# Performance work log

Measured on AMD Instinct MI355X. Metric: run time of the kernel, lower is better.

Reference implementation:

```python
import jax, jax.numpy as jnp
import numpy as np

ATT = 16          # attention_size -> window = 2*ATT+1 = 33
HID = 512         # middle hidden size


def setup_inputs() -> dict:
    key = jax.random.key(0)
    ks = jax.random.split(key, 7)
    B, S, D_IN = 4, 2048, 256
    def xav(k, shape):
        fan_in, fan_out = shape[0], shape[1]
        std = np.sqrt(2.0 / (fan_in + fan_out))
        return jax.random.normal(k, shape, dtype=jnp.float32) * std
    return {
        "x": jax.random.normal(ks[0], (B, S, D_IN), dtype=jnp.float32),
        "Wq": xav(ks[1], (HID, HID)),
        "Wk": xav(ks[2], (HID, HID)),
        "Wv": xav(ks[3], (HID, HID)),
        "W0": xav(ks[4], (D_IN, HID)),
        "b0": jnp.zeros((1, 1, HID), dtype=jnp.float32),
        "W1": xav(ks[5], (HID, HID)),
        "b1": jnp.zeros((1, 1, HID), dtype=jnp.float32),
        "Wout": xav(ks[6], (HID, 2)),
        "bout": jnp.zeros((1, 1, 2), dtype=jnp.float32),
    }


def _local_windows(h, A):
    # h: [B, S, H] -> nei: [B, S, 2A+1, H], nei[b,t,j] = h[b, t+A-j] (zero padded)
    S = h.shape[1]
    padded = jnp.pad(h, ((0, 0), (A, A), (0, 0)))
    t = jnp.arange(S)[:, None]
    j = jnp.arange(2 * A + 1)[None, :]
    idx = t + 2 * A - j  # padded index of h[t + A - j]
    return padded[:, idx, :]


def reference(x, Wq, Wk, Wv, W0, b0, W1, b1, Wout, bout):
    scale = jnp.float32(np.sqrt(float(HID)))
    # pre-attention MLP layer(s)
    h = jax.nn.relu(x @ W0 + b0)                       # [B,S,H]
    nei = _local_windows(h, ATT)                       # [B,S,W,H]
    q = h @ Wq                                         # [B,S,H]
    k = nei @ Wk                                       # [B,S,W,H]
    v = nei @ Wv                                       # [B,S,W,H]
    dist = jnp.einsum('bsd,bswd->bsw', q, k) / scale   # [B,S,W]
    attn = jax.nn.softmax(dist, axis=-1)               # [B,S,W]
    ctx = jnp.einsum('bsw,bswd->bsd', attn, v)         # [B,S,H]
    # post-attention MLP layers
    h2 = jax.nn.relu(ctx @ W1 + b1)
    out = h2 @ Wout + bout                             # [B,S,2]
    return out, attn[:, :, None, :]  # attn shape [B,S,1,W] as in torch
```

## Files before the change

kernel.cpp:

```cpp
#include <hip/hip_runtime.h>

#define S_LEN 2048
#define HID 512
#define DIN 256
#define WIN 33
#define MROWS 8192
#define VTB 2080
#define VTROW 8320
#define SCALE_INV 0.04419417382415922f

typedef __attribute__((ext_vector_type(8))) short short8;
typedef __attribute__((ext_vector_type(4))) float f32x4;

__device__ __forceinline__ unsigned short f2bf(float f) {
    unsigned u = __builtin_bit_cast(unsigned, f);
    u += 0x7fffu + ((u >> 16) & 1u);
    return (unsigned short)(u >> 16);
}
__device__ __forceinline__ float bf2f(unsigned short h) {
    unsigned u = ((unsigned)h) << 16;
    return __builtin_bit_cast(float, u);
}
__device__ __forceinline__ void gl_lds16(const unsigned short* g, unsigned short* l) {
    __builtin_amdgcn_global_load_lds(
        (__attribute__((address_space(1))) unsigned int*)(g),
        (__attribute__((address_space(3))) unsigned int*)(l),
        16, 0, 0);
}

__global__ __launch_bounds__(256) void prep_kernel(
    const float* __restrict__ x,
    const float* __restrict__ Wq, const float* __restrict__ Wk,
    const float* __restrict__ Wv, const float* __restrict__ W0,
    const float* __restrict__ W1, const float* __restrict__ bout,
    unsigned short* __restrict__ xb, unsigned short* __restrict__ Wt0,
    unsigned short* __restrict__ Wtqkv, unsigned short* __restrict__ Wt1,
    unsigned short* __restrict__ Vt, float* __restrict__ outp)
{
    __shared__ float tile[32][33];
    const int blk = blockIdx.x, tid = threadIdx.x;
    if (blk < 2048) {
        int i = (blk * 256 + tid) * 4;
        float4 v = *(const float4*)(x + i);
        unsigned lo = (unsigned)f2bf(v.x) | ((unsigned)f2bf(v.y) << 16);
        unsigned hi = (unsigned)f2bf(v.z) | ((unsigned)f2bf(v.w) << 16);
        uint2 p; p.x = lo; p.y = hi;
        *(uint2*)(xb + i) = p;
    } else if (blk < 2064) {
        int i = ((blk - 2048) * 256 + tid) * 4;
        float4 o; o.x = bout[0]; o.y = bout[1]; o.z = bout[0]; o.w = bout[1];
        *(float4*)(outp + i) = o;
    } else if (blk < 2320) {
        int t = (blk - 2064) * 256 + tid;
        int v = t >> 7, s = t & 127;
        int b = s >> 5, p = s & 31;
        int off = (p < 16) ? p : (2048 + p);
        Vt[(size_t)v * VTROW + b * VTB + off] = 0;
    } else {
        int tt = blk - 2320;
        const float* in; unsigned short* out; int K, kt, nt;
        if (tt < 128) { in = W0; out = Wt0; K = DIN; kt = tt & 7; nt = tt >> 3; }
        else {
            int z = (tt - 128) >> 8, r = (tt - 128) & 255;
            kt = r & 15; nt = r >> 4; K = HID;
            if (z == 0)      { in = Wq; out = Wtqkv; }
            else if (z == 1) { in = Wk; out = Wtqkv + 512 * 512; }
            else if (z == 2) { in = Wv; out = Wtqkv + 2 * 512 * 512; }
            else             { in = W1; out = Wt1; }
        }
        int k0 = kt * 32, n0 = nt * 32;
        int tx = tid & 31, ty = tid >> 5;
        for (int j = 0; j < 32; j += 8)
            tile[ty + j][tx] = in[(size_t)(k0 + ty + j) * HID + n0 + tx];
        __syncthreads();
        for (int j = 0; j < 32; j += 8)
            out[(size_t)(n0 + ty + j) * K + k0 + tx] = f2bf(tile[tx][ty + j]);
    }
}

template<int K, int MODE>
__global__ __launch_bounds__(256) void gemm128_kernel(
    const unsigned short* __restrict__ A,
    const unsigned short* __restrict__ Bt,
    const float* __restrict__ bias,
    unsigned short* __restrict__ C0,
    unsigned short* __restrict__ C1,
    unsigned short* __restrict__ C2,
    const float* __restrict__ Wout,
    float* __restrict__ outp)
{
    __shared__ __align__(16) unsigned short SMEM[8192];
    const int tid = threadIdx.x;
    const int lane = tid & 63, wid = tid >> 6;
    const int bn = blockIdx.x, bm = blockIdx.y;
    const int wr = wid >> 1, wc = wid & 1;
    const int r16 = lane & 15, kq = lane >> 4;

    f32x4 acc[4][4] = {};

    const int c0 = tid, c1 = tid + 256;
    const unsigned short* aS0 = A + (size_t)(bm * 128 + (c0 & 127)) * K + (c0 >> 7) * 8;
    const unsigned short* aS1 = A + (size_t)(bm * 128 + (c1 & 127)) * K + (c1 >> 7) * 8;
    const unsigned short* bS0 = Bt + (size_t)(bn * 128 + (c0 & 127)) * K + (c0 >> 7) * 8;
    const unsigned short* bS1 = Bt + (size_t)(bn * 128 + (c1 & 127)) * K + (c1 >> 7) * 8;
    unsigned short* aD0 = SMEM + c0 * 8;
    unsigned short* aD1 = SMEM + c1 * 8;
    unsigned short* bD0 = SMEM + 4096 + c0 * 8;
    unsigned short* bD1 = SMEM + 4096 + c1 * 8;

    for (int kt = 0; kt < K / 32; ++kt) {
        gl_lds16(aS0 + kt * 32, aD0);
        gl_lds16(aS1 + kt * 32, aD1);
        gl_lds16(bS0 + kt * 32, bD0);
        gl_lds16(bS1 + kt * 32, bD1);
        __syncthreads();
        short8 af[4], bfr[4];
        #pragma unroll
        for (int mi = 0; mi < 4; ++mi)
            af[mi] = *(const short8*)(SMEM + kq * 1024 + (wr * 64 + mi * 16 + r16) * 8);
        #pragma unroll
        for (int ni = 0; ni < 4; ++ni)
            bfr[ni] = *(const short8*)(SMEM + 4096 + kq * 1024 + (wc * 64 + ni * 16 + r16) * 8);
        #pragma unroll
        for (int mi = 0; mi < 4; ++mi)
            #pragma unroll
            for (int ni = 0; ni < 4; ++ni)
                acc[mi][ni] = __builtin_amdgcn_mfma_f32_16x16x32_bf16(af[mi], bfr[ni], acc[mi][ni], 0, 0, 0);
        __syncthreads();
    }

    if constexpr (MODE == 0) {
        #pragma unroll
        for (int mi = 0; mi < 4; ++mi) {
            int row0 = bm * 128 + wr * 64 + mi * 16 + kq * 4;
            #pragma unroll
            for (int ni = 0; ni < 4; ++ni) {
                int col = bn * 128 + wc * 64 + ni * 16 + r16;
                float bv = bias[col];
                #pragma unroll
                for (int r = 0; r < 4; ++r) {
                    float v = fmaxf(acc[mi][ni][r] + bv, 0.0f);
                    C0[(size_t)(row0 + r) * HID + col] = f2bf(v);
                }
            }
        }
    } else if constexpr (MODE == 1) {
        if (bn < 8) {
            unsigned short* dst = (bn < 4) ? C0 : C1;
            int cb = (bn & 3) * 128 + wc * 64;
            #pragma unroll
            for (int mi = 0; mi < 4; ++mi) {
                int row0 = bm * 128 + wr * 64 + mi * 16 + kq * 4;
                #pragma unroll
                for (int ni = 0; ni < 4; ++ni) {
                    int col = cb + ni * 16 + r16;
                    #pragma unroll
                    for (int r = 0; r < 4; ++r)
                        dst[(size_t)(row0 + r) * HID + col] = f2bf(acc[mi][ni][r]);
                }
            }
        } else {
            const int bb  = (bm * 128) >> 11;
            const int tl0 = (bm * 128) & 2047;
            #pragma unroll
            for (int p = 0; p < 2; ++p) {
                if (wc == p) {
                    #pragma unroll
                    for (int mi = 0; mi < 4; ++mi) {
                        int ttw = wr * 64 + mi * 16 + kq * 4;
                        #pragma unroll
                        for (int ni = 0; ni < 4; ++ni) {
                            int vv = ni * 16 + r16;
                            unsigned lo = (unsigned)f2bf(acc[mi][ni][0]) | ((unsigned)f2bf(acc[mi][ni][1]) << 16);
                            unsigned hi = (unsigned)f2bf(acc[mi][ni][2]) | ((unsigned)f2bf(acc[mi][ni][3]) << 16);
                            uint2 pk; pk.x = lo; pk.y = hi;
                            *(uint2*)&SMEM[vv * 128 + (ttw ^ ((vv & 7) << 3))] = pk;
                        }
                    }
                }
                __syncthreads();
                #pragma unroll
                for (int it = 0; it < 4; ++it) {
                    int vv  = (tid >> 4) + it * 16;
                    int tt8 = (tid & 15) * 8;
                    uint4 q = *(const uint4*)&SMEM[vv * 128 + (tt8 ^ ((vv & 7) << 3))];
                    int vg = (bn - 8) * 128 + p * 64 + vv;
                    *(uint4*)(C2 + (size_t)vg * VTROW + bb * VTB + 16 + tl0 + tt8) = q;
                }
                __syncthreads();
            }
        }
    } else {
        float o0[16], o1[16];
        #pragma unroll
        for (int t2 = 0; t2 < 16; ++t2) { o0[t2] = 0.0f; o1[t2] = 0.0f; }
        #pragma unroll
        for (int ni = 0; ni < 4; ++ni) {
            int col = bn * 128 + wc * 64 + ni * 16 + r16;
            float bv = bias[col];
            float2 wv = *(const float2*)(Wout + col * 2);
            #pragma unroll
            for (int mi = 0; mi < 4; ++mi)
                #pragma unroll
                for (int r = 0; r < 4; ++r) {
                    float v = fmaxf(acc[mi][ni][r] + bv, 0.0f);
                    o0[mi * 4 + r] += v * wv.x;
                    o1[mi * 4 + r] += v * wv.y;
                }
        }
        #pragma unroll
        for (int s = 1; s < 16; s <<= 1)
            #pragma unroll
            for (int t2 = 0; t2 < 16; ++t2) {
                o0[t2] += __shfl_xor(o0[t2], s);
                o1[t2] += __shfl_xor(o1[t2], s);
            }
        if (r16 == 0) {
            #pragma unroll
            for (int mi = 0; mi < 4; ++mi)
                #pragma unroll
                for (int r = 0; r < 4; ++r) {
                    int row = bm * 128 + wr * 64 + mi * 16 + kq * 4 + r;
                    atomicAdd(&outp[(size_t)row * 2],     o0[mi * 4 + r]);
                    atomicAdd(&outp[(size_t)row * 2 + 1], o1[mi * 4 + r]);
                }
        }
    }
}

__global__ __launch_bounds__(256) void attn_kernel(
    const unsigned short* __restrict__ Qb,
    const unsigned short* __restrict__ Kb,
    const unsigned short* __restrict__ Vt,
    float* __restrict__ attn_out,
    unsigned short* __restrict__ ctx)
{
    __shared__ __align__(16) float Sl[4][32][66];
    __shared__ __align__(16) unsigned short Pl[32 * 64];
    const int tid = threadIdx.x;
    const int lane = tid & 63;
    const int w = tid >> 6;
    const int t0g = blockIdx.x * 32;
    const int b = t0g >> 11;
    const int t0 = t0g & 2047;
    const int r16 = lane & 15, kq = lane >> 4;

    f32x4 s[2][4] = {};
    const unsigned short* qbase = Qb + (size_t)t0g * HID + w * 128 + kq * 8;
    const unsigned short* kbase = Kb + (long)(t0g - 16) * HID + w * 128 + kq * 8;
    #pragma unroll
    for (int ks = 0; ks < 4; ++ks) {
        short8 a0 = *(const short8*)(qbase + (size_t)r16 * HID + ks * 32);
        short8 a1 = *(const short8*)(qbase + (size_t)(16 + r16) * HID + ks * 32);
        #pragma unroll
        for (int ni = 0; ni < 4; ++ni) {
            short8 bf = *(const short8*)(kbase + (size_t)(ni * 16 + r16) * HID + ks * 32);
            s[0][ni] = __builtin_amdgcn_mfma_f32_16x16x32_bf16(a0, bf, s[0][ni], 0, 0, 0);
            s[1][ni] = __builtin_amdgcn_mfma_f32_16x16x32_bf16(a1, bf, s[1][ni], 0, 0, 0);
        }
    }
    #pragma unroll
    for (int mi = 0; mi < 2; ++mi)
        #pragma unroll
        for (int ni = 0; ni < 4; ++ni)
            #pragma unroll
            for (int r = 0; r < 4; ++r)
                Sl[w][mi * 16 + kq * 4 + r][ni * 16 + r16] = s[mi][ni][r];
    __syncthreads();

    {
        const int i = tid >> 3;
        const int c8 = (tid & 7) * 8;
        float sv[8];
        #pragma unroll
        for (int cc = 0; cc < 8; ++cc) {
            float a = Sl[0][i][c8 + cc] + Sl[1][i][c8 + cc]
                    + Sl[2][i][c8 + cc] + Sl[3][i][c8 + cc];
            int m = c8 + cc;
            bool inb = (m >= i) && (m <= i + 32);
            int krow = t0 + m - 16;
            bool inseq = (krow >= 0) && (krow < S_LEN);
            sv[cc] = inb ? (inseq ? a * SCALE_INV : 0.0f) : -INFINITY;
        }
        float mx = sv[0];
        #pragma unroll
        for (int cc = 1; cc < 8; ++cc) mx = fmaxf(mx, sv[cc]);
        mx = fmaxf(mx, __shfl_xor(mx, 1));
        mx = fmaxf(mx, __shfl_xor(mx, 2));
        mx = fmaxf(mx, __shfl_xor(mx, 4));
        float es = 0.0f;
        #pragma unroll
        for (int cc = 0; cc < 8; ++cc) { sv[cc] = __expf(sv[cc] - mx); es += sv[cc]; }
        es += __shfl_xor(es, 1);
        es += __shfl_xor(es, 2);
        es += __shfl_xor(es, 4);
        float inv = 1.0f / es;
        unsigned short pb[8];
        #pragma unroll
        for (int cc = 0; cc < 8; ++cc) {
            float p = sv[cc] * inv;
            pb[cc] = f2bf(p);
            int m = c8 + cc;
            if (m >= i && m <= i + 32)
                attn_out[(size_t)(t0g + i) * WIN + (i + 32 - m)] = p;
        }
        uint4 pk;
        pk.x = (unsigned)pb[0] | ((unsigned)pb[1] << 16);
        pk.y = (unsigned)pb[2] | ((unsigned)pb[3] << 16);
        pk.z = (unsigned)pb[4] | ((unsigned)pb[5] << 16);
        pk.w = (unsigned)pb[6] | ((unsigned)pb[7] << 16);
        *(uint4*)((char*)Pl + i * 128 + ((c8 * 2) ^ ((i & 7) << 4))) = pk;
    }
    __syncthreads();

    f32x4 c[2][8] = {};
    const char* plb = (const char*)Pl;
    const unsigned short* vtb = Vt + (size_t)b * VTB + t0;
    #pragma unroll
    for (int ks = 0; ks < 2; ++ks) {
        int cb = ks * 64 + kq * 16;
        short8 a0 = *(const short8*)(plb + r16 * 128 + (cb ^ ((r16 & 7) << 4)));
        short8 a1 = *(const short8*)(plb + (16 + r16) * 128 + (cb ^ ((r16 & 7) << 4)));
        #pragma unroll
        for (int nd = 0; nd < 8; ++nd) {
            const unsigned short* vp = vtb + (size_t)(w * 128 + nd * 16 + r16) * VTROW + ks * 32 + kq * 8;
            short8 bf = *(const short8*)vp;
            c[0][nd] = __builtin_amdgcn_mfma_f32_16x16x32_bf16(a0, bf, c[0][nd], 0, 0, 0);
            c[1][nd] = __builtin_amdgcn_mfma_f32_16x16x32_bf16(a1, bf, c[1][nd], 0, 0, 0);
        }
    }
    #pragma unroll
    for (int mi = 0; mi < 2; ++mi) {
        int row0 = t0g + mi * 16 + kq * 4;
        #pragma unroll
        for (int nd = 0; nd < 8; ++nd) {
            int col = w * 128 + nd * 16 + r16;
            #pragma unroll
            for (int r = 0; r < 4; ++r)
                ctx[(size_t)(row0 + r) * HID + col] = f2bf(c[mi][nd][r]);
        }
    }
}

extern "C" void kernel_launch(void* const* d_in, const int* in_sizes, int n_in,
                              void* d_out, int out_size, void* d_ws, size_t ws_size,
                              hipStream_t stream)
{
    const float* x    = (const float*)d_in[0];
    const float* Wq   = (const float*)d_in[1];
    const float* Wk   = (const float*)d_in[2];
    const float* Wv   = (const float*)d_in[3];
    const float* W0   = (const float*)d_in[4];
    const float* b0   = (const float*)d_in[5];
    const float* W1   = (const float*)d_in[6];
    const float* b1   = (const float*)d_in[7];
    const float* Wout = (const float*)d_in[8];
    const float* bout = (const float*)d_in[9];

    char* ws = (char*)d_ws;
    unsigned short* xb    = (unsigned short*)(ws + 0);
    unsigned short* Wt0   = (unsigned short*)(ws + (4u  << 20));
    unsigned short* Wtqkv = (unsigned short*)(ws + 4456448u);
    unsigned short* Wt1   = (unsigned short*)(ws + 6029312u);
    unsigned short* hB    = (unsigned short*)(ws + (8u  << 20));
    unsigned short* Qb    = (unsigned short*)(ws + (16u << 20));
    unsigned short* Kb    = (unsigned short*)(ws + (24u << 20));
    unsigned short* Vt    = (unsigned short*)(ws + (32u << 20));
    unsigned short* ctxB  = (unsigned short*)(ws + (41u << 20));

    float* outp  = (float*)d_out;
    float* attnp = (float*)d_out + MROWS * 2;

    prep_kernel<<<3472, 256, 0, stream>>>(x, Wq, Wk, Wv, W0, W1, bout,
                                          xb, Wt0, Wtqkv, Wt1, Vt, outp);

    gemm128_kernel<DIN, 0><<<dim3(4, 64), 256, 0, stream>>>(
        xb, Wt0, b0, hB, nullptr, nullptr, nullptr, nullptr);

    gemm128_kernel<HID, 1><<<dim3(12, 64), 256, 0, stream>>>(
        hB, Wtqkv, nullptr, Qb, Kb, Vt, nullptr, nullptr);

    attn_kernel<<<256, 256, 0, stream>>>(Qb, Kb, Vt, attnp, ctxB);

    gemm128_kernel<HID, 2><<<dim3(4, 64), 256, 0, stream>>>(
        ctxB, Wt1, b1, nullptr, nullptr, nullptr, Wout, outp);
}
```

Baseline: 154.6 us.

## Double-buffer LDS tiles in bf16 GEMM to overlap global loads with MFMA

Doubles the shared-memory tile buffer and prefetches the next K-slice with global_load_lds while the current slice feeds MFMA. Explicit vmcnt waits and raw s_barrier calls with sched_barrier fences replace the plain __syncthreads pair. The goal is to hide global-to-LDS latency behind compute. In exchange, LDS use per block doubles to 32KB, which may lower occupancy, and the hand-written waitcnt counts must match the number of outstanding loads.

```diff
diff --git a/kernel.cpp b/kernel.cpp
--- a/kernel.cpp
+++ b/kernel.cpp
@@ -89,12 +89,13 @@
     const float* __restrict__ Wout,
     float* __restrict__ outp)
 {
-    __shared__ __align__(16) unsigned short SMEM[8192];
+    __shared__ __align__(16) unsigned short SMEM[16384];
     const int tid = threadIdx.x;
     const int lane = tid & 63, wid = tid >> 6;
     const int bn = blockIdx.x, bm = blockIdx.y;
     const int wr = wid >> 1, wc = wid & 1;
     const int r16 = lane & 15, kq = lane >> 4;
+    const int NT = K / 32;
 
     f32x4 acc[4][4] = {};
 
@@ -103,31 +104,48 @@
     const unsigned short* aS1 = A + (size_t)(bm * 128 + (c1 & 127)) * K + (c1 >> 7) * 8;
     const unsigned short* bS0 = Bt + (size_t)(bn * 128 + (c0 & 127)) * K + (c0 >> 7) * 8;
     const unsigned short* bS1 = Bt + (size_t)(bn * 128 + (c1 & 127)) * K + (c1 >> 7) * 8;
-    unsigned short* aD0 = SMEM + c0 * 8;
-    unsigned short* aD1 = SMEM + c1 * 8;
-    unsigned short* bD0 = SMEM + 4096 + c0 * 8;
-    unsigned short* bD1 = SMEM + 4096 + c1 * 8;
-
-    for (int kt = 0; kt < K / 32; ++kt) {
-        gl_lds16(aS0 + kt * 32, aD0);
-        gl_lds16(aS1 + kt * 32, aD1);
-        gl_lds16(bS0 + kt * 32, bD0);
-        gl_lds16(bS1 + kt * 32, bD1);
-        __syncthreads();
+
+    #define STAGE(buf, kt) do { \
+        gl_lds16(aS0 + (kt) * 32, SMEM + (buf) * 8192 + c0 * 8); \
+        gl_lds16(aS1 + (kt) * 32, SMEM + (buf) * 8192 + c1 * 8); \
+        gl_lds16(bS0 + (kt) * 32, SMEM + (buf) * 8192 + 4096 + c0 * 8); \
+        gl_lds16(bS1 + (kt) * 32, SMEM + (buf) * 8192 + 4096 + c1 * 8); \
+    } while (0)
+
+    STAGE(0, 0);
+    for (int kt = 0; kt < NT; ++kt) {
+        const int cur = kt & 1;
+        if (kt + 1 < NT) {
+            STAGE(cur ^ 1, kt + 1);
+            asm volatile("s_waitcnt vmcnt(4)" ::: "memory");
+        } else {
+            asm volatile("s_waitcnt vmcnt(0)" ::: "memory");
+        }
+        __builtin_amdgcn_sched_barrier(0);
+        __builtin_amdgcn_s_barrier();
+        __builtin_amdgcn_sched_barrier(0);
+
+        const unsigned short* ab = SMEM + cur * 8192;
+        const unsigned short* bb = ab + 4096;
         short8 af[4], bfr[4];
         #pragma unroll
         for (int mi = 0; mi < 4; ++mi)
-            af[mi] = *(const short8*)(SMEM + kq * 1024 + (wr * 64 + mi * 16 + r16) * 8);
+            af[mi] = *(const short8*)(ab + kq * 1024 + (wr * 64 + mi * 16 + r16) * 8);
         #pragma unroll
         for (int ni = 0; ni < 4; ++ni)
-            bfr[ni] = *(const short8*)(SMEM + 4096 + kq * 1024 + (wc * 64 + ni * 16 + r16) * 8);
+            bfr[ni] = *(const short8*)(bb + kq * 1024 + (wc * 64 + ni * 16 + r16) * 8);
         #pragma unroll
         for (int mi = 0; mi < 4; ++mi)
             #pragma unroll
             for (int ni = 0; ni < 4; ++ni)
                 acc[mi][ni] = __builtin_amdgcn_mfma_f32_16x16x32_bf16(af[mi], bfr[ni], acc[mi][ni], 0, 0, 0);
-        __syncthreads();
-    }
+
+        asm volatile("s_waitcnt lgkmcnt(0)" ::: "memory");
+        __builtin_amdgcn_sched_barrier(0);
+        __builtin_amdgcn_s_barrier();
+        __builtin_amdgcn_sched_barrier(0);
+    }
+    #undef STAGE
 
     if constexpr (MODE == 0) {
         #pragma unroll
```

New measurement: 147.8 us. 4.4% less time.
